# Kernel optimization log

Measured on AMD Instinct MI355X. Metric: run time of the kernel, lower is better.

The kernel has to match this reference:

```python
import jax, jax.numpy as jnp
import numpy as np

N_NODES = 100000
N_EDGES = 1600000
IN_DIM, HID_DIM, OUT_DIM = 64, 64, 16


def setup_inputs() -> dict:
    key = jax.random.key(0)
    k1, k2, k3, k4 = jax.random.split(key, 4)
    x = jax.random.normal(k1, (N_NODES, IN_DIM), dtype=jnp.float32)
    edge_index = jax.random.randint(k2, (2, N_EDGES), 0, N_NODES, dtype=jnp.int64)
    W1 = jax.random.normal(k3, (IN_DIM, HID_DIM), dtype=jnp.float32) * (1.0 / np.sqrt(IN_DIM))
    b1 = jnp.zeros((HID_DIM,), dtype=jnp.float32)
    W2 = jax.random.normal(k4, (HID_DIM, OUT_DIM), dtype=jnp.float32) * (1.0 / np.sqrt(HID_DIM))
    b2 = jnp.zeros((OUT_DIM,), dtype=jnp.float32)
    return {"x": x, "edge_index": edge_index, "W1": W1, "b1": b1, "W2": W2, "b2": b2}


def gcn_conv(x, src, dst, W, b, num_nodes):
    """GCNConv: h = D^{-1/2} (A+I) D^{-1/2} (x W) + b, edge-list form with self-loops already appended."""
    # symmetric degree normalization (degree counted at destination, incl. self-loops)
    deg = jax.ops.segment_sum(jnp.ones_like(dst, dtype=x.dtype), dst, num_segments=num_nodes)
    dinv = jnp.where(deg > 0, jax.lax.rsqrt(deg), 0.0)
    norm = dinv[src] * dinv[dst]                      # [E+N]
    h = x @ W                                         # [N, H] project first (fewer flops on edges)
    msg = h[src] * norm[:, None]                      # gather + scale, [E+N, H]
    out = jax.ops.segment_sum(msg, dst, num_segments=num_nodes)  # scatter-add
    return out + b


def reference(x, edge_index, W1, b1, W2, b2):
    num_nodes = x.shape[0]
    loop = jnp.arange(num_nodes, dtype=edge_index.dtype)
    src = jnp.concatenate([edge_index[0], loop])      # add self-loops once, reuse for both layers
    dst = jnp.concatenate([edge_index[1], loop])
    h = gcn_conv(x, src, dst, W1, b1, num_nodes)
    h = jax.nn.relu(h)
    # F.dropout(training=self.training): eval mode -> identity
    out = gcn_conv(h, src, dst, W2, b2, num_nodes)
    return out
```

## Files before the change

kernel.cpp:

```cpp
#include <hip/hip_runtime.h>

constexpr int N_NODES = 100000;
constexpr int F1 = 64;
constexpr int F2 = 16;
constexpr int NPB = 128;
constexpr int NBINS = (N_NODES + NPB - 1) / NPB;
constexpr int CAPB = 2560;
constexpr int TILE = 4096;

static __device__ __forceinline__ unsigned short f2bf(float f) {
    unsigned int u = __float_as_uint(f);
    unsigned int r = (u + 0x7fffu + ((u >> 16) & 1u)) >> 16;
    return (unsigned short)r;
}
static __device__ __forceinline__ float bf2f(unsigned short b) {
    return __uint_as_float(((unsigned int)b) << 16);
}

__global__ __launch_bounds__(256) void k_bin(const int* __restrict__ src,
                                             const int* __restrict__ dst, int E,
                                             unsigned int* __restrict__ gcnt,
                                             unsigned int* __restrict__ entries) {
    __shared__ unsigned int cnt[NBINS];
    __shared__ unsigned int cur[NBINS];
    int tid = threadIdx.x;
    int base = blockIdx.x * TILE;
    int end = min(base + TILE, E);
    for (int i = tid; i < NBINS; i += 256) cnt[i] = 0;
    __syncthreads();
    for (int e = base + tid; e < end; e += 256) {
        int b = dst[e] >> 7;
        atomicAdd(&cnt[b], 1u);
    }
    __syncthreads();
    for (int i = tid; i < NBINS; i += 256) {
        unsigned int c = cnt[i];
        cur[i] = (unsigned int)i * CAPB + (c ? atomicAdd(&gcnt[i], c) : 0u);
    }
    __syncthreads();
    for (int e = base + tid; e < end; e += 256) {
        int d = dst[e];
        int s = src[e];
        int b = d >> 7;
        unsigned int p = atomicAdd(&cur[b], 1u);
        if (p - (unsigned int)b * CAPB < CAPB)
            entries[p] = (unsigned int)s | ((unsigned int)(d & 127) << 17);
    }
}

__global__ __launch_bounds__(256) void k_dinvb(const unsigned int* __restrict__ gcnt,
                                               const unsigned int* __restrict__ entries,
                                               float* __restrict__ dinv) {
    __shared__ unsigned int ncnt[NPB];
    int tid = threadIdx.x;
    int b = blockIdx.x;
    unsigned int cntE = gcnt[b]; if (cntE > CAPB) cntE = CAPB;
    unsigned int base = (unsigned int)b * CAPB;
    if (tid < NPB) ncnt[tid] = 0;
    __syncthreads();
    for (unsigned int e = tid; e < cntE; e += 256)
        atomicAdd(&ncnt[entries[base + e] >> 17], 1u);
    __syncthreads();
    if (tid < NPB) {
        int node = b * NPB + tid;
        if (node < N_NODES) dinv[node] = rsqrtf((float)(ncnt[tid] + 1u));
    }
}

__global__ __launch_bounds__(256) void k_xw1(const float* __restrict__ x,
                                             const float* __restrict__ W,
                                             const float* __restrict__ dinv,
                                             unsigned short* __restrict__ hs) {
    constexpr int XS = 68;
    __shared__ float Ws[64 * 64];
    __shared__ float xs[64 * XS];
    int tid = threadIdx.x;
    int r0 = blockIdx.x * 64;
    for (int i = tid; i < 1024; i += 256) {
        int k = i >> 4, c4 = (i & 15) << 2;
        *(float4*)&Ws[k * 64 + c4] = *(const float4*)&W[k * 64 + c4];
    }
    for (int i = tid; i < 1024; i += 256) {
        int rr = i >> 4, c4 = (i & 15) << 2;
        int r = r0 + rr;
        float4 v = make_float4(0.f, 0.f, 0.f, 0.f);
        if (r < N_NODES) v = *(const float4*)&x[(size_t)r * 64 + c4];
        *(float4*)&xs[rr * XS + c4] = v;
    }
    __syncthreads();
    int tx = tid & 15, ty = tid >> 4;
    int c0 = tx << 2;
    int rb = ty << 2;
    float acc[4][4] = {};
#pragma unroll 8
    for (int k = 0; k < 64; ++k) {
        float4 w = *(float4*)&Ws[k * 64 + c0];
        float x0 = xs[(rb + 0) * XS + k];
        float x1 = xs[(rb + 1) * XS + k];
        float x2 = xs[(rb + 2) * XS + k];
        float x3 = xs[(rb + 3) * XS + k];
        acc[0][0] += x0 * w.x; acc[0][1] += x0 * w.y; acc[0][2] += x0 * w.z; acc[0][3] += x0 * w.w;
        acc[1][0] += x1 * w.x; acc[1][1] += x1 * w.y; acc[1][2] += x1 * w.z; acc[1][3] += x1 * w.w;
        acc[2][0] += x2 * w.x; acc[2][1] += x2 * w.y; acc[2][2] += x2 * w.z; acc[2][3] += x2 * w.w;
        acc[3][0] += x3 * w.x; acc[3][1] += x3 * w.y; acc[3][2] += x3 * w.z; acc[3][3] += x3 * w.w;
    }
#pragma unroll
    for (int i = 0; i < 4; ++i) {
        int r = r0 + rb + i;
        if (r >= N_NODES) break;
        float dv = dinv[r];
        ushort4 p;
        p.x = f2bf(acc[i][0] * dv);
        p.y = f2bf(acc[i][1] * dv);
        p.z = f2bf(acc[i][2] * dv);
        p.w = f2bf(acc[i][3] * dv);
        *(ushort4*)&hs[(size_t)r * 64 + c0] = p;
    }
}

__global__ __launch_bounds__(1024) void k_agg1f(const unsigned int* __restrict__ gcnt,
                                                const unsigned int* __restrict__ entries,
                                                const unsigned short* __restrict__ hs,
                                                const float* __restrict__ dinv,
                                                unsigned short* __restrict__ out1) {
    __shared__ unsigned int ncnt[NPB];
    __shared__ unsigned int noff[NPB + 1];
    __shared__ unsigned int cur[NPB];
    __shared__ unsigned int sl[CAPB];
    int tid = threadIdx.x;
    int b = blockIdx.x;
    unsigned int cntE = gcnt[b]; if (cntE > CAPB) cntE = CAPB;
    unsigned int base = (unsigned int)b * CAPB;
    if (tid < NPB) ncnt[tid] = 0;
    __syncthreads();
    for (unsigned int e = tid; e < cntE; e += 1024)
        atomicAdd(&ncnt[entries[base + e] >> 17], 1u);
    __syncthreads();
    if (tid < NPB) cur[tid] = ncnt[tid];
    __syncthreads();
    for (int ofs = 1; ofs < NPB; ofs <<= 1) {
        unsigned int v = (tid < NPB && tid >= ofs) ? cur[tid - ofs] : 0u;
        __syncthreads();
        if (tid < NPB) cur[tid] += v;
        __syncthreads();
    }
    if (tid < NPB) noff[tid + 1] = cur[tid];
    if (tid == 0) noff[0] = 0;
    __syncthreads();
    if (tid < NPB) cur[tid] = noff[tid];
    __syncthreads();
    for (unsigned int e = tid; e < cntE; e += 1024) {
        unsigned int v = entries[base + e];
        unsigned int p = atomicAdd(&cur[v >> 17], 1u);
        sl[p] = v & 0x1FFFFu;
    }
    __syncthreads();
    int wid = tid >> 6, k = tid & 63;
    for (int n = wid; n < NPB; n += 16) {
        int node = b * NPB + n;
        if (node >= N_NODES) break;
        unsigned int j = noff[n], jend = noff[n + 1];
        float acc = bf2f(hs[(size_t)node * 64 + k]);
        for (; j + 8 <= jend; j += 8) {
            unsigned int s0 = sl[j], s1 = sl[j + 1], s2 = sl[j + 2], s3 = sl[j + 3];
            unsigned int s4 = sl[j + 4], s5 = sl[j + 5], s6 = sl[j + 6], s7 = sl[j + 7];
            float a0 = bf2f(hs[(size_t)s0 * 64 + k]);
            float a1 = bf2f(hs[(size_t)s1 * 64 + k]);
            float a2 = bf2f(hs[(size_t)s2 * 64 + k]);
            float a3 = bf2f(hs[(size_t)s3 * 64 + k]);
            float a4 = bf2f(hs[(size_t)s4 * 64 + k]);
            float a5 = bf2f(hs[(size_t)s5 * 64 + k]);
            float a6 = bf2f(hs[(size_t)s6 * 64 + k]);
            float a7 = bf2f(hs[(size_t)s7 * 64 + k]);
            acc += ((a0 + a1) + (a2 + a3)) + ((a4 + a5) + (a6 + a7));
        }
        for (; j + 4 <= jend; j += 4) {
            unsigned int s0 = sl[j], s1 = sl[j + 1], s2 = sl[j + 2], s3 = sl[j + 3];
            float a0 = bf2f(hs[(size_t)s0 * 64 + k]);
            float a1 = bf2f(hs[(size_t)s1 * 64 + k]);
            float a2 = bf2f(hs[(size_t)s2 * 64 + k]);
            float a3 = bf2f(hs[(size_t)s3 * 64 + k]);
            acc += (a0 + a1) + (a2 + a3);
        }
        for (; j < jend; ++j) acc += bf2f(hs[(size_t)sl[j] * 64 + k]);
        out1[(size_t)node * 64 + k] = f2bf(acc * dinv[node]);
    }
}

__global__ __launch_bounds__(256) void k_xw2(const unsigned short* __restrict__ out1,
                                             const float* __restrict__ b1,
                                             const float* __restrict__ W2,
                                             const float* __restrict__ dinv,
                                             unsigned short* __restrict__ h2s) {
    constexpr int RS = 66;
    __shared__ float Ws[64 * 16];
    __shared__ float rs[128 * RS];
    __shared__ float b1s[64];
    int tid = threadIdx.x;
    int r0 = blockIdx.x * 128;
    if (tid < 64) b1s[tid] = b1[tid];
    for (int i = tid; i < 256; i += 256)
        *(float4*)&Ws[i * 4] = *(const float4*)&W2[i * 4];
    __syncthreads();
    for (int i = tid; i < 2048; i += 256) {
        int rr = i >> 4, c4 = (i & 15) << 2;
        int r = r0 + rr;
        float v0 = 0.f, v1 = 0.f, v2 = 0.f, v3 = 0.f;
        if (r < N_NODES) {
            ushort4 u = *(const ushort4*)&out1[(size_t)r * 64 + c4];
            v0 = fmaxf(bf2f(u.x) + b1s[c4 + 0], 0.f);
            v1 = fmaxf(bf2f(u.y) + b1s[c4 + 1], 0.f);
            v2 = fmaxf(bf2f(u.z) + b1s[c4 + 2], 0.f);
            v3 = fmaxf(bf2f(u.w) + b1s[c4 + 3], 0.f);
        }
        float* p = &rs[rr * RS + c4];
        p[0] = v0; p[1] = v1; p[2] = v2; p[3] = v3;
    }
    __syncthreads();
    int tx = tid & 3, ty = tid >> 2;
    int c0 = tx << 2;
    int rb = ty << 1;
    float acc[2][4] = {};
#pragma unroll 8
    for (int k = 0; k < 64; ++k) {
        float4 w = *(float4*)&Ws[k * 16 + c0];
        float x0 = rs[(rb + 0) * RS + k];
        float x1 = rs[(rb + 1) * RS + k];
        acc[0][0] += x0 * w.x; acc[0][1] += x0 * w.y; acc[0][2] += x0 * w.z; acc[0][3] += x0 * w.w;
        acc[1][0] += x1 * w.x; acc[1][1] += x1 * w.y; acc[1][2] += x1 * w.z; acc[1][3] += x1 * w.w;
    }
#pragma unroll
    for (int i = 0; i < 2; ++i) {
        int r = r0 + rb + i;
        if (r >= N_NODES) break;
        float dv = dinv[r];
        ushort4 p;
        p.x = f2bf(acc[i][0] * dv);
        p.y = f2bf(acc[i][1] * dv);
        p.z = f2bf(acc[i][2] * dv);
        p.w = f2bf(acc[i][3] * dv);
        *(ushort4*)&h2s[(size_t)r * 16 + c0] = p;
    }
}

__global__ __launch_bounds__(1024) void k_agg2f(const unsigned int* __restrict__ gcnt,
                                                const unsigned int* __restrict__ entries,
                                                const unsigned short* __restrict__ h2s,
                                                const float* __restrict__ dinv,
                                                const float* __restrict__ b2,
                                                float* __restrict__ out) {
    __shared__ unsigned int ncnt[NPB];
    __shared__ unsigned int noff[NPB + 1];
    __shared__ unsigned int cur[NPB];
    __shared__ unsigned int sl[CAPB];
    int tid = threadIdx.x;
    int b = blockIdx.x;
    unsigned int cntE = gcnt[b]; if (cntE > CAPB) cntE = CAPB;
    unsigned int base = (unsigned int)b * CAPB;
    if (tid < NPB) ncnt[tid] = 0;
    __syncthreads();
    for (unsigned int e = tid; e < cntE; e += 1024)
        atomicAdd(&ncnt[entries[base + e] >> 17], 1u);
    __syncthreads();
    if (tid < NPB) cur[tid] = ncnt[tid];
    __syncthreads();
    for (int ofs = 1; ofs < NPB; ofs <<= 1) {
        unsigned int v = (tid < NPB && tid >= ofs) ? cur[tid - ofs] : 0u;
        __syncthreads();
        if (tid < NPB) cur[tid] += v;
        __syncthreads();
    }
    if (tid < NPB) noff[tid + 1] = cur[tid];
    if (tid == 0) noff[0] = 0;
    __syncthreads();
    if (tid < NPB) cur[tid] = noff[tid];
    __syncthreads();
    for (unsigned int e = tid; e < cntE; e += 1024) {
        unsigned int v = entries[base + e];
        unsigned int p = atomicAdd(&cur[v >> 17], 1u);
        sl[p] = v & 0x1FFFFu;
    }
    __syncthreads();
    int wid = tid >> 6, lane = tid & 63;
    int k = lane & 15, esub = lane >> 4;
    for (int n = wid; n < NPB; n += 16) {
        int node = b * NPB + n;
        if (node >= N_NODES) break;
        unsigned int j0 = noff[n], jend = noff[n + 1];
        float acc = 0.0f;
        unsigned int j = j0 + esub;
        for (; j + 4 < jend; j += 8) {
            float a = bf2f(h2s[(size_t)sl[j] * 16 + k]);
            float c = bf2f(h2s[(size_t)sl[j + 4] * 16 + k]);
            acc += a + c;
        }
        if (j < jend) acc += bf2f(h2s[(size_t)sl[j] * 16 + k]);
        acc += __shfl_xor(acc, 16);
        acc += __shfl_xor(acc, 32);
        if (lane < 16)
            out[(size_t)node * 16 + k] = (acc + bf2f(h2s[(size_t)node * 16 + k])) * dinv[node] + b2[k];
    }
}

static inline size_t align256(size_t x) { return (x + 255) & ~size_t(255); }

extern "C" void kernel_launch(void* const* d_in, const int* in_sizes, int n_in,
                              void* d_out, int out_size, void* d_ws, size_t ws_size,
                              hipStream_t stream) {
    const float* x  = (const float*)d_in[0];
    const int* edge = (const int*)d_in[1];
    const float* W1 = (const float*)d_in[2];
    const float* b1 = (const float*)d_in[3];
    const float* W2 = (const float*)d_in[4];
    const float* b2 = (const float*)d_in[5];
    float* out = (float*)d_out;

    const int E = in_sizes[1] / 2;
    const int* src = edge;
    const int* dst = edge + E;

    char* ws = (char*)d_ws;
    size_t o = 0;
    unsigned int* gcnt    = (unsigned int*)(ws + o); o += align256((size_t)NBINS * 4);
    float* dinv           = (float*)(ws + o);        o += align256((size_t)N_NODES * 4);
    unsigned int* entries = (unsigned int*)(ws + o); o += align256((size_t)NBINS * CAPB * 4);
    unsigned short* hs    = (unsigned short*)(ws + o); o += align256((size_t)N_NODES * F1 * 2);
    unsigned short* out1  = (unsigned short*)(ws + o); o += align256((size_t)N_NODES * F1 * 2);
    unsigned short* h2s   = (unsigned short*)(ws + o); o += align256((size_t)N_NODES * F2 * 2);

    hipMemsetAsync(gcnt, 0, (size_t)NBINS * 4, stream);

    k_bin<<<(E + TILE - 1) / TILE, 256, 0, stream>>>(src, dst, E, gcnt, entries);
    k_dinvb<<<NBINS, 256, 0, stream>>>(gcnt, entries, dinv);

    k_xw1<<<(N_NODES + 63) / 64, 256, 0, stream>>>(x, W1, dinv, hs);
    k_agg1f<<<NBINS, 1024, 0, stream>>>(gcnt, entries, hs, dinv, out1);

    k_xw2<<<(N_NODES + 127) / 128, 256, 0, stream>>>(out1, b1, W2, dinv, h2s);
    k_agg2f<<<NBINS, 1024, 0, stream>>>(gcnt, entries, h2s, dinv, b2, out);
}
```

Baseline: 148.1 us.

## Build per-bin CSR once in degree kernel and reuse it in both aggregations

The degree kernel now also runs the per-bin prefix scan and counting sort, writing sorted source lists and node offsets to global memory. Both aggregation kernels read that CSR instead of re-sorting the entries in shared memory each time. This removes duplicated sort work and LDS use. The aggregation kernels drop to 512 threads, layer 1 processes two nodes per wave in an interleaved loop, and layer 2 uses a predicated strided loop. The cost is an extra global sorted array and offset table that must be written once and read back twice.

```diff
diff --git a/kernel.cpp b/kernel.cpp
--- a/kernel.cpp
+++ b/kernel.cpp
@@ -3,6 +3,7 @@
 constexpr int N_NODES = 100000;
 constexpr int F1 = 64;
 constexpr int F2 = 16;
+constexpr int SH = 7;
 constexpr int NPB = 128;
 constexpr int NBINS = (N_NODES + NPB - 1) / NPB;
 constexpr int CAPB = 2560;
@@ -28,10 +29,7 @@
     int end = min(base + TILE, E);
     for (int i = tid; i < NBINS; i += 256) cnt[i] = 0;
     __syncthreads();
-    for (int e = base + tid; e < end; e += 256) {
-        int b = dst[e] >> 7;
-        atomicAdd(&cnt[b], 1u);
-    }
+    for (int e = base + tid; e < end; e += 256) atomicAdd(&cnt[dst[e] >> SH], 1u);
     __syncthreads();
     for (int i = tid; i < NBINS; i += 256) {
         unsigned int c = cnt[i];
@@ -41,17 +39,21 @@
     for (int e = base + tid; e < end; e += 256) {
         int d = dst[e];
         int s = src[e];
-        int b = d >> 7;
-        unsigned int p = atomicAdd(&cur[b], 1u);
-        if (p - (unsigned int)b * CAPB < CAPB)
-            entries[p] = (unsigned int)s | ((unsigned int)(d & 127) << 17);
-    }
-}
-
-__global__ __launch_bounds__(256) void k_dinvb(const unsigned int* __restrict__ gcnt,
-                                               const unsigned int* __restrict__ entries,
-                                               float* __restrict__ dinv) {
+        int bb = d >> SH;
+        unsigned int p = atomicAdd(&cur[bb], 1u);
+        if (p - (unsigned int)bb * CAPB < CAPB)
+            entries[p] = (unsigned int)s | ((unsigned int)(d & (NPB - 1)) << 17);
+    }
+}
+
+__global__ __launch_bounds__(256) void k_csr(const unsigned int* __restrict__ gcnt,
+                                             const unsigned int* __restrict__ entries,
+                                             unsigned int* __restrict__ noffg,
+                                             unsigned int* __restrict__ sorted,
+                                             float* __restrict__ dinv) {
     __shared__ unsigned int ncnt[NPB];
+    __shared__ unsigned int noff[NPB + 1];
+    __shared__ unsigned int cur[NPB];
     int tid = threadIdx.x;
     int b = blockIdx.x;
     unsigned int cntE = gcnt[b]; if (cntE > CAPB) cntE = CAPB;
@@ -61,10 +63,29 @@
     for (unsigned int e = tid; e < cntE; e += 256)
         atomicAdd(&ncnt[entries[base + e] >> 17], 1u);
     __syncthreads();
+    if (tid < NPB) cur[tid] = ncnt[tid];
+    __syncthreads();
+    for (int ofs = 1; ofs < NPB; ofs <<= 1) {
+        unsigned int v = (tid < NPB && tid >= ofs) ? cur[tid - ofs] : 0u;
+        __syncthreads();
+        if (tid < NPB) cur[tid] += v;
+        __syncthreads();
+    }
+    if (tid < NPB) noff[tid + 1] = cur[tid];
+    if (tid == 0) noff[0] = 0;
+    __syncthreads();
     if (tid < NPB) {
         int node = b * NPB + tid;
         if (node < N_NODES) dinv[node] = rsqrtf((float)(ncnt[tid] + 1u));
-    }
+        cur[tid] = noff[tid];
+    }
+    __syncthreads();
+    for (unsigned int e = tid; e < cntE; e += 256) {
+        unsigned int v = entries[base + e];
+        unsigned int p = atomicAdd(&cur[v >> 17], 1u);
+        sorted[base + p] = v & 0x1FFFFu;
+    }
+    if (tid <= NPB) noffg[b * (NPB + 1) + tid] = noff[tid];
 }
 
 __global__ __launch_bounds__(256) void k_xw1(const float* __restrict__ x,
@@ -89,8 +110,7 @@
     }
     __syncthreads();
     int tx = tid & 15, ty = tid >> 4;
-    int c0 = tx << 2;
-    int rb = ty << 2;
+    int c0 = tx << 2, rb = ty << 2;
     float acc[4][4] = {};
 #pragma unroll 8
     for (int k = 0; k < 64; ++k) {
@@ -118,72 +138,71 @@
     }
 }
 
-__global__ __launch_bounds__(1024) void k_agg1f(const unsigned int* __restrict__ gcnt,
-                                                const unsigned int* __restrict__ entries,
-                                                const unsigned short* __restrict__ hs,
-                                                const float* __restrict__ dinv,
-                                                unsigned short* __restrict__ out1) {
-    __shared__ unsigned int ncnt[NPB];
-    __shared__ unsigned int noff[NPB + 1];
-    __shared__ unsigned int cur[NPB];
-    __shared__ unsigned int sl[CAPB];
+__global__ __launch_bounds__(512) void k_agg1f(const unsigned int* __restrict__ noffg,
+                                               const unsigned int* __restrict__ sorted,
+                                               const unsigned short* __restrict__ hs,
+                                               const float* __restrict__ dinv,
+                                               unsigned short* __restrict__ out1) {
+    __shared__ unsigned int noffs[NPB + 1];
     int tid = threadIdx.x;
     int b = blockIdx.x;
-    unsigned int cntE = gcnt[b]; if (cntE > CAPB) cntE = CAPB;
+    if (tid <= NPB) noffs[tid] = noffg[b * (NPB + 1) + tid];
+    __syncthreads();
     unsigned int base = (unsigned int)b * CAPB;
-    if (tid < NPB) ncnt[tid] = 0;
-    __syncthreads();
-    for (unsigned int e = tid; e < cntE; e += 1024)
-        atomicAdd(&ncnt[entries[base + e] >> 17], 1u);
-    __syncthreads();
-    if (tid < NPB) cur[tid] = ncnt[tid];
-    __syncthreads();
-    for (int ofs = 1; ofs < NPB; ofs <<= 1) {
-        unsigned int v = (tid < NPB && tid >= ofs) ? cur[tid - ofs] : 0u;
-        __syncthreads();
-        if (tid < NPB) cur[tid] += v;
-        __syncthreads();
-    }
-    if (tid < NPB) noff[tid + 1] = cur[tid];
-    if (tid == 0) noff[0] = 0;
-    __syncthreads();
-    if (tid < NPB) cur[tid] = noff[tid];
-    __syncthreads();
-    for (unsigned int e = tid; e < cntE; e += 1024) {
-        unsigned int v = entries[base + e];
-        unsigned int p = atomicAdd(&cur[v >> 17], 1u);
-        sl[p] = v & 0x1FFFFu;
-    }
-    __syncthreads();
-    int wid = tid >> 6, k = tid & 63;
-    for (int n = wid; n < NPB; n += 16) {
-        int node = b * NPB + n;
-        if (node >= N_NODES) break;
-        unsigned int j = noff[n], jend = noff[n + 1];
-        float acc = bf2f(hs[(size_t)node * 64 + k]);
-        for (; j + 8 <= jend; j += 8) {
-            unsigned int s0 = sl[j], s1 = sl[j + 1], s2 = sl[j + 2], s3 = sl[j + 3];
-            unsigned int s4 = sl[j + 4], s5 = sl[j + 5], s6 = sl[j + 6], s7 = sl[j + 7];
-            float a0 = bf2f(hs[(size_t)s0 * 64 + k]);
-            float a1 = bf2f(hs[(size_t)s1 * 64 + k]);
-            float a2 = bf2f(hs[(size_t)s2 * 64 + k]);
-            float a3 = bf2f(hs[(size_t)s3 * 64 + k]);
-            float a4 = bf2f(hs[(size_t)s4 * 64 + k]);
-            float a5 = bf2f(hs[(size_t)s5 * 64 + k]);
-            float a6 = bf2f(hs[(size_t)s6 * 64 + k]);
-            float a7 = bf2f(hs[(size_t)s7 * 64 + k]);
-            acc += ((a0 + a1) + (a2 + a3)) + ((a4 + a5) + (a6 + a7));
-        }
-        for (; j + 4 <= jend; j += 4) {
-            unsigned int s0 = sl[j], s1 = sl[j + 1], s2 = sl[j + 2], s3 = sl[j + 3];
-            float a0 = bf2f(hs[(size_t)s0 * 64 + k]);
-            float a1 = bf2f(hs[(size_t)s1 * 64 + k]);
-            float a2 = bf2f(hs[(size_t)s2 * 64 + k]);
-            float a3 = bf2f(hs[(size_t)s3 * 64 + k]);
-            acc += (a0 + a1) + (a2 + a3);
-        }
-        for (; j < jend; ++j) acc += bf2f(hs[(size_t)sl[j] * 64 + k]);
-        out1[(size_t)node * 64 + k] = f2bf(acc * dinv[node]);
+    int wv = tid >> 6, k = tid & 63;
+#pragma unroll 1
+    for (int p = 0; p < 8; ++p) {
+        int nA = (wv << 4) + (p << 1);
+        int nB = nA + 1;
+        int nodeA = b * NPB + nA;
+        if (nodeA >= N_NODES) break;
+        int nodeB = nodeA + 1;
+        bool hasB = nodeB < N_NODES;
+        unsigned int jA = noffs[nA], eA = noffs[nA + 1];
+        unsigned int jB = noffs[nB], eB = noffs[nB + 1];
+        float accA = bf2f(hs[(size_t)nodeA * 64 + k]);
+        float accB = hasB ? bf2f(hs[(size_t)nodeB * 64 + k]) : 0.f;
+        while (jA + 4 <= eA && jB + 4 <= eB) {
+            unsigned int a0 = sorted[base + jA], a1 = sorted[base + jA + 1];
+            unsigned int a2 = sorted[base + jA + 2], a3 = sorted[base + jA + 3];
+            unsigned int b0 = sorted[base + jB], b1 = sorted[base + jB + 1];
+            unsigned int b2 = sorted[base + jB + 2], b3 = sorted[base + jB + 3];
+            float va0 = bf2f(hs[(size_t)a0 * 64 + k]);
+            float va1 = bf2f(hs[(size_t)a1 * 64 + k]);
+            float va2 = bf2f(hs[(size_t)a2 * 64 + k]);
+            float va3 = bf2f(hs[(size_t)a3 * 64 + k]);
+            float vb0 = bf2f(hs[(size_t)b0 * 64 + k]);
+            float vb1 = bf2f(hs[(size_t)b1 * 64 + k]);
+            float vb2 = bf2f(hs[(size_t)b2 * 64 + k]);
+            float vb3 = bf2f(hs[(size_t)b3 * 64 + k]);
+            accA += (va0 + va1) + (va2 + va3);
+            accB += (vb0 + vb1) + (vb2 + vb3);
+            jA += 4; jB += 4;
+        }
+        while (jA + 4 <= eA) {
+            unsigned int a0 = sorted[base + jA], a1 = sorted[base + jA + 1];
+            unsigned int a2 = sorted[base + jA + 2], a3 = sorted[base + jA + 3];
+            float va0 = bf2f(hs[(size_t)a0 * 64 + k]);
+            float va1 = bf2f(hs[(size_t)a1 * 64 + k]);
+            float va2 = bf2f(hs[(size_t)a2 * 64 + k]);
+            float va3 = bf2f(hs[(size_t)a3 * 64 + k]);
+            accA += (va0 + va1) + (va2 + va3);
+            jA += 4;
+        }
+        while (jA < eA) { accA += bf2f(hs[(size_t)sorted[base + jA] * 64 + k]); ++jA; }
+        while (jB + 4 <= eB) {
+            unsigned int b0 = sorted[base + jB], b1 = sorted[base + jB + 1];
+            unsigned int b2 = sorted[base + jB + 2], b3 = sorted[base + jB + 3];
+            float vb0 = bf2f(hs[(size_t)b0 * 64 + k]);
+            float vb1 = bf2f(hs[(size_t)b1 * 64 + k]);
+            float vb2 = bf2f(hs[(size_t)b2 * 64 + k]);
+            float vb3 = bf2f(hs[(size_t)b3 * 64 + k]);
+            accB += (vb0 + vb1) + (vb2 + vb3);
+            jB += 4;
+        }
+        while (jB < eB) { accB += bf2f(hs[(size_t)sorted[base + jB] * 64 + k]); ++jB; }
+        out1[(size_t)nodeA * 64 + k] = f2bf(accA * dinv[nodeA]);
+        if (hasB) out1[(size_t)nodeB * 64 + k] = f2bf(accB * dinv[nodeB]);
     }
 }
 
@@ -213,13 +232,12 @@
             v2 = fmaxf(bf2f(u.z) + b1s[c4 + 2], 0.f);
             v3 = fmaxf(bf2f(u.w) + b1s[c4 + 3], 0.f);
         }
-        float* p = &rs[rr * RS + c4];
-        p[0] = v0; p[1] = v1; p[2] = v2; p[3] = v3;
+        float* pp = &rs[rr * RS + c4];
+        pp[0] = v0; pp[1] = v1; pp[2] = v2; pp[3] = v3;
     }
     __syncthreads();
     int tx = tid & 3, ty = tid >> 2;
-    int c0 = tx << 2;
-    int rb = ty << 1;
+    int c0 = tx << 2, rb = ty << 1;
     float acc[2][4] = {};
 #pragma unroll 8
     for (int k = 0; k < 64; ++k) {
@@ -243,62 +261,39 @@
     }
 }
 
-__global__ __launch_bounds__(1024) void k_agg2f(const unsigned int* __restrict__ gcnt,
-                                                const unsigned int* __restrict__ entries,
-                                                const unsigned short* __restrict__ h2s,
-                                                const float* __restrict__ dinv,
-                                                const float* __restrict__ b2,
-                                                float* __restrict__ out) {
-    __shared__ unsigned int ncnt[NPB];
-    __shared__ unsigned int noff[NPB + 1];
-    __shared__ unsigned int cur[NPB];
-    __shared__ unsigned int sl[CAPB];
+__global__ __launch_bounds__(512) void k_agg2f(const unsigned int* __restrict__ noffg,
+                                               const unsigned int* __restrict__ sorted,
+                                               const unsigned short* __restrict__ h2s,
+                                               const float* __restrict__ dinv,
+                                               const float* __restrict__ b2,
+                                               float* __restrict__ out) {
+    __shared__ unsigned int noffs[NPB + 1];
+    __shared__ float b2s[16];
     int tid = threadIdx.x;
     int b = blockIdx.x;
-    unsigned int cntE = gcnt[b]; if (cntE > CAPB) cntE = CAPB;
+    if (tid <= NPB) noffs[tid] = noffg[b * (NPB + 1) + tid];
+    if (tid >= 128 && tid < 144) b2s[tid - 128] = b2[tid - 128];
+    __syncthreads();
     unsigned int base = (unsigned int)b * CAPB;
-    if (tid < NPB) ncnt[tid] = 0;
-    __syncthreads();
-    for (unsigned int e = tid; e < cntE; e += 1024)
-        atomicAdd(&ncnt[entries[base + e] >> 17], 1u);
-    __syncthreads();
-    if (tid < NPB) cur[tid] = ncnt[tid];
-    __syncthreads();
-    for (int ofs = 1; ofs < NPB; ofs <<= 1) {
-        unsigned int v = (tid < NPB && tid >= ofs) ? cur[tid - ofs] : 0u;
-        __syncthreads();
-        if (tid < NPB) cur[tid] += v;
-        __syncthreads();
-    }
-    if (tid < NPB) noff[tid + 1] = cur[tid];
-    if (tid == 0) noff[0] = 0;
-    __syncthreads();
-    if (tid < NPB) cur[tid] = noff[tid];
-    __syncthreads();
-    for (unsigned int e = tid; e < cntE; e += 1024) {
-        unsigned int v = entries[base + e];
-        unsigned int p = atomicAdd(&cur[v >> 17], 1u);
-        sl[p] = v & 0x1FFFFu;
-    }
-    __syncthreads();
-    int wid = tid >> 6, lane = tid & 63;
-    int k = lane & 15, esub = lane >> 4;
-    for (int n = wid; n < NPB; n += 16) {
+    int wv = tid >> 6, lane = tid & 63;
+    int k = lane & 15, slot = lane >> 4;
+    for (int p = 0; p < 16; ++p) {
+        int n = (wv << 4) + p;
         int node = b * NPB + n;
         if (node >= N_NODES) break;
-        unsigned int j0 = noff[n], jend = noff[n + 1];
-        float acc = 0.0f;
-        unsigned int j = j0 + esub;
-        for (; j + 4 < jend; j += 8) {
-            float a = bf2f(h2s[(size_t)sl[j] * 16 + k]);
-            float c = bf2f(h2s[(size_t)sl[j + 4] * 16 + k]);
-            acc += a + c;
-        }
-        if (j < jend) acc += bf2f(h2s[(size_t)sl[j] * 16 + k]);
+        unsigned int j0 = noffs[n], jend = noffs[n + 1];
+        float acc = 0.f;
+        for (unsigned int j = j0; j < jend; j += 8) {
+            unsigned int i1 = j + (unsigned)slot;
+            unsigned int i2 = i1 + 4;
+            float v1 = (i1 < jend) ? bf2f(h2s[(size_t)sorted[base + i1] * 16 + k]) : 0.f;
+            float v2 = (i2 < jend) ? bf2f(h2s[(size_t)sorted[base + i2] * 16 + k]) : 0.f;
+            acc += v1 + v2;
+        }
         acc += __shfl_xor(acc, 16);
         acc += __shfl_xor(acc, 32);
         if (lane < 16)
-            out[(size_t)node * 16 + k] = (acc + bf2f(h2s[(size_t)node * 16 + k])) * dinv[node] + b2[k];
+            out[(size_t)node * 16 + k] = (acc + bf2f(h2s[(size_t)node * 16 + k])) * dinv[node] + b2s[k];
     }
 }
 
@@ -324,6 +319,8 @@
     unsigned int* gcnt    = (unsigned int*)(ws + o); o += align256((size_t)NBINS * 4);
     float* dinv           = (float*)(ws + o);        o += align256((size_t)N_NODES * 4);
     unsigned int* entries = (unsigned int*)(ws + o); o += align256((size_t)NBINS * CAPB * 4);
+    unsigned int* sorted  = (unsigned int*)(ws + o); o += align256((size_t)NBINS * CAPB * 4);
+    unsigned int* noffg   = (unsigned int*)(ws + o); o += align256((size_t)NBINS * (NPB + 1) * 4);
     unsigned short* hs    = (unsigned short*)(ws + o); o += align256((size_t)N_NODES * F1 * 2);
     unsigned short* out1  = (unsigned short*)(ws + o); o += align256((size_t)N_NODES * F1 * 2);
     unsigned short* h2s   = (unsigned short*)(ws + o); o += align256((size_t)N_NODES * F2 * 2);
@@ -331,11 +328,11 @@
     hipMemsetAsync(gcnt, 0, (size_t)NBINS * 4, stream);
 
     k_bin<<<(E + TILE - 1) / TILE, 256, 0, stream>>>(src, dst, E, gcnt, entries);
-    k_dinvb<<<NBINS, 256, 0, stream>>>(gcnt, entries, dinv);
+    k_csr<<<NBINS, 256, 0, stream>>>(gcnt, entries, noffg, sorted, dinv);
 
     k_xw1<<<(N_NODES + 63) / 64, 256, 0, stream>>>(x, W1, dinv, hs);
-    k_agg1f<<<NBINS, 1024, 0, stream>>>(gcnt, entries, hs, dinv, out1);
+    k_agg1f<<<NBINS, 512, 0, stream>>>(noffg, sorted, hs, dinv, out1);
 
     k_xw2<<<(N_NODES + 127) / 128, 256, 0, stream>>>(out1, b1, W2, dinv, h2s);
-    k_agg2f<<<NBINS, 1024, 0, stream>>>(gcnt, entries, h2s, dinv, b2, out);
-}
+    k_agg2f<<<NBINS, 512, 0, stream>>>(noffg, sorted, h2s, dinv, b2, out);
+}
```

After: 185.4 us. 1.25x slower.
